# Optimization experiments

Hardware: AMD Instinct MI355X
Metric: run time of the kernel (lower is better)

The kernel has to match this reference:

```python
import jax, jax.numpy as jnp
import numpy as np
import math

K = 3
K2 = 9
BANDS = 8

def _linear(x, w, b):
    return x @ w.T + b

def _gelu(x):
    return jax.nn.gelu(x, approximate=False)

def setup_inputs() -> dict:
    key = jax.random.key(0)
    ks = jax.random.split(key, 14)
    def p(k, shape):
        return jax.random.normal(k, shape, dtype=jnp.float32) * 0.05
    inp = {
        "feat": jax.random.normal(ks[0], (2, 64, 128, 128), dtype=jnp.float32),
        "w1m": p(ks[1], (64, 85)),  "b1m": p(ks[2], (64,)),
        "w2m": p(ks[3], (64, 64)),  "b2m": p(ks[4], (64,)),
        "wk1": p(ks[5], (128, 640)), "bk1": p(ks[6], (128,)),
        "wk2": p(ks[7], (9, 128)),   "bk2": p(ks[8], (9,)),
        "wr1": p(ks[9], (64, 64)),   "br1": p(ks[10], (64,)),
        "wr2": p(ks[11], (3, 64)),   "br2": p(ks[12], (3,)),
        "scale": 2,
    }
    return inp

def reference(feat, w1m, b1m, w2m, b2m, wk1, bk1, wk2, bk2, wr1, br1, wr2, br2, scale):
    B, C, H, W = feat.shape
    s = float(scale)
    oh = max(1, int(round(H * s)))
    ow = max(1, int(round(W * s)))
    kappa = max(0.1, 1.0 / s)
    eta = min(1.0, 0.15 * s)
    pad = K // 2

    # ---- query geometry (shared across batch: uniform scale) ----
    ys = jnp.arange(oh, dtype=feat.dtype)
    xs = jnp.arange(ow, dtype=feat.dtype)
    yy, xx = jnp.meshgrid(ys, xs, indexing='ij')
    src_y = (yy + 0.5) / s - 0.5
    src_x = (xx + 0.5) / s - 0.5
    cell_y = jnp.floor(src_y)
    cell_x = jnp.floor(src_x)
    du = (src_x - cell_x - 0.5).reshape(-1)  # (q,)
    dv = (src_y - cell_y - 0.5).reshape(-1)
    q = oh * ow

    # ---- gather local KxK patches (replicates unfold + index_select) ----
    cy = jnp.clip(cell_y, 0, H - 1).astype(jnp.int32).reshape(-1)
    cx = jnp.clip(cell_x, 0, W - 1).astype(jnp.int32).reshape(-1)
    padded = jnp.pad(feat, ((0, 0), (0, 0), (pad, pad), (pad, pad)), mode='reflect')
    off = jnp.arange(K, dtype=jnp.int32)
    rows = cy[:, None] + off                 # (q, K) -> padded row indices
    cols = cx[:, None] + off                 # (q, K)
    # (B, C, q, K, K)
    g = padded[:, :, rows[:, :, None], cols[:, None, :]]
    g = jnp.transpose(g, (0, 2, 1, 3, 4)).reshape(B, q, C * K2)  # torch unfold layout (c, kh, kw)
    # torch does gathered.view(q, k2, c) on the channel-major flat -> faithful reshape
    patches = g.reshape(B, q, K2, C)
    patches_flat = g  # (B, q, C*K2), identical to patches.reshape(q, -1)

    # ---- meta fourier encoding + meta MLP (shared across batch) ----
    m = jnp.stack([
        jnp.full((q,), s, dtype=feat.dtype),
        du, dv,
        jnp.full((q,), kappa, dtype=feat.dtype),
        jnp.full((q,), eta, dtype=feat.dtype),
    ], axis=1)                               # (q, 5)
    freqs = (2.0 ** jnp.arange(BANDS, dtype=feat.dtype)) * math.pi
    xb = m[..., None] * freqs                # (q, 5, BANDS)
    enc = jnp.concatenate([m[..., None], jnp.sin(xb), jnp.cos(xb)], axis=-1).reshape(q, -1)  # (q, 85)
    m_emb = _linear(_gelu(_linear(enc, w1m, b1m)), w2m, b2m)  # (q, channels)

    # ---- kernel generation + softmax-weighted aggregate ----
    m_emb_b = jnp.broadcast_to(m_emb[None], (B, q, m_emb.shape[-1]))
    kin = jnp.concatenate([patches_flat, m_emb_b], axis=-1)   # (B, q, 640)
    weights = _linear(_gelu(_linear(kin, wk1, bk1)), wk2, bk2)  # (B, q, K2)
    weights = jax.nn.softmax(weights, axis=-1)
    f_q = jnp.einsum('bqk,bqkc->bqc', weights, patches)       # (B, q, C)

    # ---- rgb head ----
    rgb = _linear(_gelu(_linear(f_q, wr1, br1)), wr2, br2)    # (B, q, 3)
    rgb = rgb.reshape(B, oh, ow, -1).transpose(0, 3, 1, 2)    # (B, 3, oh, ow)
    return rgb
```

## Files before the change

### kernel.cpp

```cpp
#include <hip/hip_runtime.h>
#include <math.h>

#define HH 128
#define WW 128

typedef __attribute__((ext_vector_type(8))) short s16x8;
typedef __attribute__((ext_vector_type(8))) _Float16 h16x8;
typedef __attribute__((ext_vector_type(4))) float f32x4;

__device__ __forceinline__ float gelu_f(float x){
    return 0.5f * x * (1.0f + erff(x * 0.70710678118654752440f));
}
__device__ __forceinline__ float gelu2(float x){
    const float u2 = 1.5957691216057308f * x * (1.0f + 0.044715f * x * x);
    const float e  = __expf(u2);
    const float t  = 1.0f - 2.0f * __builtin_amdgcn_rcpf(e + 1.0f);
    return 0.5f * x * (1.0f + t);
}
__device__ __forceinline__ int refl(int v, int n){
    return v < 0 ? -v : (v >= n ? 2*n - 2 - v : v);
}
__device__ __forceinline__ ushort f2bf(float f){
    unsigned int b = __float_as_uint(f);
    unsigned int r = (b + 0x7FFFu + ((b >> 16) & 1u)) >> 16;
    return (ushort)r;
}
__device__ __forceinline__ float bf2f(ushort u){
    return __uint_as_float(((unsigned int)u) << 16);
}

__global__ __launch_bounds__(256) void featTp_kernel(
    const float* __restrict__ feat, ushort* __restrict__ featTp)
{
    __shared__ ushort tile[64*132];

    const int blk = blockIdx.x;
    const int b   = blk / 130;
    const int row = blk - b*130;
    const int sr  = refl(row - 1, HH);

    const int c2   = threadIdx.x >> 7;
    const int scol = threadIdx.x & 127;

    #pragma unroll 4
    for (int cc = 0; cc < 32; ++cc){
        const int c = cc*2 + c2;
        const float v = feat[(((size_t)(b*64 + c)) << 14) + (sr << 7) + scol];
        const ushort bv = f2bf(v);
        tile[c*132 + scol + 1] = bv;
        if (scol == 1)   tile[c*132 + 0]   = bv;
        if (scol == 126) tile[c*132 + 129] = bv;
    }
    __syncthreads();

    for (int e = threadIdx.x; e < 1040; e += 256){
        const int col = e >> 3;
        const int cb  = e & 7;
        ushort tmp[8];
        #pragma unroll
        for (int j = 0; j < 8; ++j) tmp[j] = tile[(cb*8 + j)*132 + col];
        *(int4*)(featTp + ((((size_t)b*130 + row)*130 + col) << 6) + cb*8)
            = *(const int4*)tmp;
    }
}

__global__ __launch_bounds__(256) void prep_all(
    const float* __restrict__ w1m, const float* __restrict__ b1m,
    const float* __restrict__ w2m, const float* __restrict__ b2m,
    const float* __restrict__ wk1, const float* __restrict__ bk1,
    const float* __restrict__ wr1,
    float* __restrict__ contrib, ushort* __restrict__ wk1tap,
    _Float16* __restrict__ wr1h)
{
    const int blk = blockIdx.x;
    const int t = threadIdx.x;

    if (blk == 0){
        __shared__ float hs[4][64];
        __shared__ float m_emb[4][64];
        const int p = t >> 6;
        const int j = t & 63;

        const float du = (p & 1) ? -0.25f : 0.25f;
        const float dv = (p >> 1) ? -0.25f : 0.25f;
        const float mv[5] = {2.0f, du, dv, 0.5f, 0.3f};

        float enc[85];
        #pragma unroll
        for (int f = 0; f < 5; ++f){
            enc[f*17] = mv[f];
            float fr = 3.14159265358979323846f;
            #pragma unroll
            for (int b = 0; b < 8; ++b){
                float xb = mv[f] * fr;
                enc[f*17 + 1 + b] = sinf(xb);
                enc[f*17 + 9 + b] = cosf(xb);
                fr *= 2.0f;
            }
        }

        float h = b1m[j];
        const float* __restrict__ wrow = w1m + j*85;
        #pragma unroll
        for (int i = 0; i < 85; ++i) h += enc[i] * wrow[i];
        hs[p][j] = gelu_f(h);
        __syncthreads();

        {
            const int o = j;
            float acc = b2m[o];
            const float* __restrict__ w2row = w2m + o*64;
            #pragma unroll
            for (int jj = 0; jj < 64; ++jj) acc += hs[p][jj] * w2row[jj];
            m_emb[p][o] = acc;
        }
        __syncthreads();

        for (int e = t; e < 512; e += 256){
            const int pp = e >> 7;
            const int oo = e & 127;
            float a = bk1[oo];
            #pragma unroll
            for (int jj = 0; jj < 64; ++jj) a += m_emb[pp][jj] * wk1[oo*640 + 576 + jj];
            contrib[e] = a;
        }
    } else if (blk <= 288){
        const int i = (blk - 1)*256 + t;
        if (i < 73728){
            const int c   = i & 63;
            const int o   = (i >> 6) & 127;
            const int tap = i >> 13;
            wk1tap[i] = f2bf(wk1[o*640 + c*9 + tap]);
        }
    } else {
        const int i = (blk - 289)*256 + t;
        if (i < 8192) wr1h[i] = (_Float16)wr1[i];
    }
}

__global__ __launch_bounds__(512) void conv_kernel(
    const ushort* __restrict__ featTp,
    const ushort* __restrict__ wk1tap,
    const float* __restrict__ wk2, const float* __restrict__ bk2,
    const float* __restrict__ contrib,
    _Float16* __restrict__ fqh)
{
    __shared__ ushort As[4*34*64];
    __shared__ ushort Ls16[64*130];
    __shared__ float  wk2t[128*12];
    __shared__ float  w9s[256*10];
    __shared__ float  contribs[512];

    const int t   = threadIdx.x;
    const int blk = blockIdx.x;
    const int b   = blk >> 8;
    const int rem = blk & 255;
    const int cy0 = (rem >> 2) * 2;
    const int cx0 = (rem & 3) * 32;

    for (int e = t; e < 1088; e += 512){
        const int r   = e / 272;
        const int rm  = e - r * 272;
        const int col = rm >> 3;
        const int cb  = rm & 7;
        const ushort* src = featTp + ((((size_t)b*130 + cy0 + r)*130 + cx0 + col) << 6) + cb*8;
        const int didx = (r*34 + col)*64 + ((cb ^ (col & 7)) << 3);
        *(int4*)&As[didx] = *(const int4*)src;
    }
    for (int e = t; e < 1536; e += 512){
        const int o = (e * 10923) >> 17;
        const int k = e - o*12;
        if (k < 9) wk2t[e] = wk2[k*128 + o];
    }
    if (t < 512) contribs[t] = contrib[t];
    __syncthreads();

    {
        const int lane = t & 63;
        const int w    = t >> 6;
        const int wn   = w & 1;
        const int wq   = w >> 1;
        const int cellrow = wq >> 1;
        const int colblk  = (wq & 1) * 16;
        const int l15  = lane & 15;
        const int l4   = lane >> 4;

        f32x4 acc[4];
        #pragma unroll
        for (int n = 0; n < 4; ++n) acc[n] = (f32x4){0.f,0.f,0.f,0.f};

        const int acol = colblk + l15;

        #pragma unroll
        for (int tap = 0; tap < 9; ++tap){
            const int ky = tap / 3;
            const int kx = tap - ky * 3;

            s16x8 bf[2][4];
            #pragma unroll
            for (int ks = 0; ks < 2; ++ks)
                #pragma unroll
                for (int n = 0; n < 4; ++n)
                    bf[ks][n] = *(const s16x8*)(wk1tap +
                        (((size_t)tap << 13) + ((wn*64 + n*16 + l15) << 6) + ks*32 + l4*8));

            const int col = acol + kx;
            const int rowbase = (cellrow + ky)*34 + col;
            const int sw = (col & 7);
            #pragma unroll
            for (int ks = 0; ks < 2; ++ks){
                const int cb0 = ks*4 + l4;
                const s16x8 af = *(const s16x8*)&As[rowbase*64 + ((cb0 ^ sw) << 3)];
                #pragma unroll
                for (int n = 0; n < 4; ++n)
                    acc[n] = __builtin_amdgcn_mfma_f32_16x16x32_bf16(af, bf[ks][n], acc[n], 0, 0, 0);
            }
        }

        #pragma unroll
        for (int n = 0; n < 4; ++n){
            #pragma unroll
            for (int reg = 0; reg < 4; ++reg){
                const int lc = cellrow*32 + colblk + l4*4 + reg;
                const int o  = wn*64 + n*16 + l15;
                Ls16[lc*130 + o] = __builtin_bit_cast(ushort, (_Float16)acc[n][reg]);
            }
        }
    }
    __syncthreads();

    if (t < 256){
        const int cell = t & 63;
        const int p    = t >> 6;

        float w9[9];
        #pragma unroll
        for (int k = 0; k < 9; ++k) w9[k] = 0.0f;

        const float* __restrict__ cp = contribs + p*128;
        for (int o = 0; o < 128; ++o){
            const float lv = (float)__builtin_bit_cast(_Float16, Ls16[cell*130 + o]);
            const float h  = gelu2(lv + cp[o]);
            const f32x4 wa = *(const f32x4*)&wk2t[o*12];
            const f32x4 wb = *(const f32x4*)&wk2t[o*12 + 4];
            w9[0] += h*wa[0]; w9[1] += h*wa[1]; w9[2] += h*wa[2]; w9[3] += h*wa[3];
            w9[4] += h*wb[0]; w9[5] += h*wb[1]; w9[6] += h*wb[2]; w9[7] += h*wb[3];
            w9[8] += h*wk2t[o*12 + 8];
        }
        #pragma unroll
        for (int k = 0; k < 9; ++k) w9[k] += bk2[k];

        float mx = w9[0];
        #pragma unroll
        for (int k = 1; k < 9; ++k) mx = fmaxf(mx, w9[k]);
        float sum = 0.0f;
        #pragma unroll
        for (int k = 0; k < 9; ++k){ w9[k] = __expf(w9[k] - mx); sum += w9[k]; }
        const float inv = __builtin_amdgcn_rcpf(sum);
        #pragma unroll
        for (int k = 0; k < 9; ++k) w9s[t*10 + k] = w9[k] * inv;
    }
    __syncthreads();

    {
        const int ci  = t >> 3;
        const int sub = t & 7;
        const int rr  = ci >> 5;
        const int x   = ci & 31;
        const int base_rc = rr*34 + x;
        const int c0 = sub*8;

        float w9r[4][9];
        #pragma unroll
        for (int p = 0; p < 4; ++p)
            #pragma unroll
            for (int k = 0; k < 9; ++k)
                w9r[p][k] = w9s[(p*64 + ci)*10 + k];

        float fqa[4][8];
        #pragma unroll
        for (int p = 0; p < 4; ++p)
            #pragma unroll
            for (int i = 0; i < 8; ++i) fqa[p][i] = 0.0f;

        #pragma unroll
        for (int k = 0; k < 9; ++k){
            #pragma unroll
            for (int i = 0; i < 8; ++i){
                const int e   = k*64 + c0 + i;
                const int ch  = (e * 7282) >> 16;
                const int tap = e - 9*ch;
                const int ty  = (tap * 11) >> 5;
                const int tx  = tap - 3*ty;
                const int col = x + tx;
                const int aidx = ((base_rc + ty*34 + tx) << 6)
                               + (((ch >> 3) ^ (col & 7)) << 3) + (ch & 7);
                const float v = bf2f(As[aidx]);
                fqa[0][i] += w9r[0][k] * v;
                fqa[1][i] += w9r[1][k] * v;
                fqa[2][i] += w9r[2][k] * v;
                fqa[3][i] += w9r[3][k] * v;
            }
        }

        const int gy = cy0 + rr;
        const int gx = cx0 + x;

        #pragma unroll
        for (int p = 0; p < 4; ++p){
            const int py = p >> 1, px = p & 1;
            h16x8 hv;
            #pragma unroll
            for (int i = 0; i < 8; ++i) hv[i] = (_Float16)fqa[p][i];

            const int oy0 = 2*gy + 2 - py;
            const int ox0 = 2*gx + 2 - px;
            const bool y0ok = (py == 1) || (gy < 127);
            const bool x0ok = (px == 1) || (gx < 127);
            const bool yEx  = (gy == 0) && (py == 0);
            const bool xEx  = (gx == 0) && (px == 0);

            if (y0ok && x0ok)
                *(h16x8*)(fqh + (((size_t)((b << 16) | (oy0 << 8) | ox0)) << 6) + c0) = hv;
            if (y0ok && xEx)
                *(h16x8*)(fqh + (((size_t)((b << 16) | (oy0 << 8))) << 6) + c0) = hv;
            if (yEx && x0ok)
                *(h16x8*)(fqh + (((size_t)((b << 16) | ox0)) << 6) + c0) = hv;
            if (yEx && xEx)
                *(h16x8*)(fqh + (((size_t)(b << 16)) << 6) + c0) = hv;
        }
    }
}

__global__ __launch_bounds__(256) void rgb_kernel(
    const _Float16* __restrict__ fqh,
    const _Float16* __restrict__ wr1h,
    const float* __restrict__ br1, const float* __restrict__ wr2,
    const float* __restrict__ br2,
    float* __restrict__ out)
{
    const int t    = threadIdx.x;
    const int w    = t >> 6;
    const int lane = t & 63;
    const int l15  = lane & 15;
    const int l4   = lane >> 4;
    const int rowbase = blockIdx.x*64 + w*16;

    const h16x8 a0 = *(const h16x8*)&fqh[(size_t)(rowbase + l15)*64 + l4*8];
    const h16x8 a1 = *(const h16x8*)&fqh[(size_t)(rowbase + l15)*64 + 32 + l4*8];

    f32x4 acc[4];
    #pragma unroll
    for (int n = 0; n < 4; ++n){
        const h16x8 b0 = *(const h16x8*)&wr1h[(n*16 + l15)*64 + l4*8];
        const h16x8 b1 = *(const h16x8*)&wr1h[(n*16 + l15)*64 + 32 + l4*8];
        acc[n] = (f32x4){0.f,0.f,0.f,0.f};
        acc[n] = __builtin_amdgcn_mfma_f32_16x16x32_f16(a0, b0, acc[n], 0, 0, 0);
        acc[n] = __builtin_amdgcn_mfma_f32_16x16x32_f16(a1, b1, acc[n], 0, 0, 0);
    }

    f32x4 br1v, wv0, wv1, wv2;
    #pragma unroll
    for (int n = 0; n < 4; ++n){
        const int col = n*16 + l15;
        br1v[n] = br1[col];
        wv0[n]  = wr2[col];
        wv1[n]  = wr2[64 + col];
        wv2[n]  = wr2[128 + col];
    }
    const float b2r0 = br2[0], b2r1 = br2[1], b2r2 = br2[2];

    #pragma unroll
    for (int reg = 0; reg < 4; ++reg){
        float r0 = 0.f, r1 = 0.f, r2 = 0.f;
        #pragma unroll
        for (int n = 0; n < 4; ++n){
            const float h = gelu2(acc[n][reg] + br1v[n]);
            r0 += h * wv0[n];
            r1 += h * wv1[n];
            r2 += h * wv2[n];
        }
        r0 += __shfl_xor(r0, 1); r0 += __shfl_xor(r0, 2); r0 += __shfl_xor(r0, 4); r0 += __shfl_xor(r0, 8);
        r1 += __shfl_xor(r1, 1); r1 += __shfl_xor(r1, 2); r1 += __shfl_xor(r1, 4); r1 += __shfl_xor(r1, 8);
        r2 += __shfl_xor(r2, 1); r2 += __shfl_xor(r2, 2); r2 += __shfl_xor(r2, 4); r2 += __shfl_xor(r2, 8);

        if (l15 == 0){
            const int row = rowbase + l4*4 + reg;
            const int b   = row >> 16;
            const int pix = row & 65535;
            out[((size_t)(b*3 + 0) << 16) + pix] = r0 + b2r0;
            out[((size_t)(b*3 + 1) << 16) + pix] = r1 + b2r1;
            out[((size_t)(b*3 + 2) << 16) + pix] = r2 + b2r2;
        }
    }
}

__global__ __launch_bounds__(256) void main_kernel_mono(
    const float* __restrict__ feat,
    const float* __restrict__ wk1,
    const float* __restrict__ wk2, const float* __restrict__ bk2,
    const float* __restrict__ wr1, const float* __restrict__ br1,
    const float* __restrict__ wr2, const float* __restrict__ br2,
    const float* __restrict__ contrib,
    float* __restrict__ out)
{
    const int tid = blockIdx.x * 256 + threadIdx.x;
    const int b  = tid >> 16;
    const int qi = tid & 65535;
    const int oy = qi >> 8;
    const int ox = qi & 255;

    int cy = (oy - 1) >> 1; if (cy < 0) cy = 0;
    int cx = (ox - 1) >> 1; if (cx < 0) cx = 0;

    int ry[3], rx[3];
    #pragma unroll
    for (int k = 0; k < 3; ++k){ ry[k] = refl(cy-1+k, HH); rx[k] = refl(cx-1+k, WW); }

    const int p = ((oy & 1) << 1) | (ox & 1);
    const float* __restrict__ fb = feat + ((size_t)b << 20);

    float w9[9];
    #pragma unroll
    for (int k = 0; k < 9; ++k) w9[k] = bk2[k];

    for (int oc = 0; oc < 4; ++oc){
        float acc[32];
        #pragma unroll
        for (int j = 0; j < 32; ++j) acc[j] = contrib[p*128 + oc*32 + j];
        for (int c = 0; c < 64; ++c){
            const float* __restrict__ fc = fb + c * (HH*WW);
            float v[9];
            #pragma unroll
            for (int ky = 0; ky < 3; ++ky){
                const float* __restrict__ frow = fc + ry[ky] * WW;
                #pragma unroll
                for (int kx = 0; kx < 3; ++kx) v[ky*3 + kx] = frow[rx[kx]];
            }
            const float* __restrict__ wrow0 = wk1 + (oc*32) * 640 + c * 9;
            #pragma unroll
            for (int j = 0; j < 32; ++j){
                const float* __restrict__ wrow = wrow0 + j * 640;
                float a = acc[j];
                #pragma unroll
                for (int kk = 0; kk < 9; ++kk) a += v[kk] * wrow[kk];
                acc[j] = a;
            }
        }
        #pragma unroll
        for (int j = 0; j < 32; ++j){
            const float h = gelu_f(acc[j]);
            const int o = oc*32 + j;
            #pragma unroll
            for (int k = 0; k < 9; ++k) w9[k] += h * wk2[k*128 + o];
        }
    }

    float mx = w9[0];
    #pragma unroll
    for (int k = 1; k < 9; ++k) mx = fmaxf(mx, w9[k]);
    float sum = 0.0f;
    #pragma unroll
    for (int k = 0; k < 9; ++k){ w9[k] = expf(w9[k] - mx); sum += w9[k]; }
    const float inv = 1.0f / sum;
    #pragma unroll
    for (int k = 0; k < 9; ++k) w9[k] *= inv;

    float fq[64];
    #pragma unroll
    for (int c = 0; c < 64; ++c){
        float a = 0.0f;
        #pragma unroll
        for (int k = 0; k < 9; ++k){
            const int j  = k*64 + c;
            const int ch = j / 9;
            const int kk = j % 9;
            a += w9[k] * fb[ch*(HH*WW) + ry[kk/3]*WW + rx[kk%3]];
        }
        fq[c] = a;
    }

    float r0 = br2[0], r1 = br2[1], r2 = br2[2];
    for (int o = 0; o < 64; ++o){
        float a = br1[o];
        #pragma unroll
        for (int c = 0; c < 64; ++c) a += fq[c] * wr1[o*64 + c];
        const float h = gelu_f(a);
        r0 += h * wr2[o];
        r1 += h * wr2[64 + o];
        r2 += h * wr2[128 + o];
    }

    const int pix = (oy << 8) | ox;
    out[((size_t)(b*3 + 0) << 16) + pix] = r0;
    out[((size_t)(b*3 + 1) << 16) + pix] = r1;
    out[((size_t)(b*3 + 2) << 16) + pix] = r2;
}

extern "C" void kernel_launch(void* const* d_in, const int* in_sizes, int n_in,
                              void* d_out, int out_size, void* d_ws, size_t ws_size,
                              hipStream_t stream)
{
    const float* feat = (const float*)d_in[0];
    const float* w1m  = (const float*)d_in[1];
    const float* b1m  = (const float*)d_in[2];
    const float* w2m  = (const float*)d_in[3];
    const float* b2m  = (const float*)d_in[4];
    const float* wk1  = (const float*)d_in[5];
    const float* bk1  = (const float*)d_in[6];
    const float* wk2  = (const float*)d_in[7];
    const float* bk2  = (const float*)d_in[8];
    const float* wr1  = (const float*)d_in[9];
    const float* br1  = (const float*)d_in[10];
    const float* wr2  = (const float*)d_in[11];
    const float* br2  = (const float*)d_in[12];

    float* out = (float*)d_out;

    char* ws = (char*)d_ws;
    float*     contrib = (float*)ws;
    ushort*    wk1tap  = (ushort*)(ws + 8192);
    _Float16*  wr1h    = (_Float16*)(ws + 155648);
    ushort*    featTp  = (ushort*)(ws + 172032);
    _Float16*  fqh     = (_Float16*)(ws + 4498432);
    const size_t need = 21275648;

    hipLaunchKernelGGL(prep_all, dim3(321), dim3(256), 0, stream,
                       w1m, b1m, w2m, b2m, wk1, bk1, wr1, contrib, wk1tap, wr1h);

    if (ws_size >= need){
        hipLaunchKernelGGL(featTp_kernel, dim3(260), dim3(256), 0, stream, feat, featTp);
        hipLaunchKernelGGL(conv_kernel, dim3(512), dim3(512), 0, stream,
                           featTp, wk1tap, wk2, bk2, contrib, fqh);
        hipLaunchKernelGGL(rgb_kernel, dim3(2048), dim3(256), 0, stream,
                           fqh, wr1h, br1, wr2, br2, out);
    } else {
        hipLaunchKernelGGL(main_kernel_mono, dim3(512), dim3(256), 0, stream,
                           feat, wk1, wk2, bk2, wr1, br1, wr2, br2, contrib, out);
    }
}
```

Measured before the change: 184.2 us.

## Merge feature transpose into prep kernel and halve conv tile per block

Folds the bf16 feature transpose into the prep_all launch as extra blocks, so one kernel launch and one dependency step go away. The conv kernel now covers 2x16 cells per block instead of 2x32, doubling the grid to 1024 blocks. The per-cell kernel-weight MLP is split across four threads per cell, with the partial sums combined by shuffles. Smaller tiles raise parallelism and occupancy through lower LDS use, but reload more halo and weights per output and add shuffle work.

```diff
diff --git a/kernel.cpp b/kernel.cpp
--- a/kernel.cpp
+++ b/kernel.cpp
@@ -29,49 +29,15 @@
     return __uint_as_float(((unsigned int)u) << 16);
 }
 
-__global__ __launch_bounds__(256) void featTp_kernel(
-    const float* __restrict__ feat, ushort* __restrict__ featTp)
-{
-    __shared__ ushort tile[64*132];
-
-    const int blk = blockIdx.x;
-    const int b   = blk / 130;
-    const int row = blk - b*130;
-    const int sr  = refl(row - 1, HH);
-
-    const int c2   = threadIdx.x >> 7;
-    const int scol = threadIdx.x & 127;
-
-    #pragma unroll 4
-    for (int cc = 0; cc < 32; ++cc){
-        const int c = cc*2 + c2;
-        const float v = feat[(((size_t)(b*64 + c)) << 14) + (sr << 7) + scol];
-        const ushort bv = f2bf(v);
-        tile[c*132 + scol + 1] = bv;
-        if (scol == 1)   tile[c*132 + 0]   = bv;
-        if (scol == 126) tile[c*132 + 129] = bv;
-    }
-    __syncthreads();
-
-    for (int e = threadIdx.x; e < 1040; e += 256){
-        const int col = e >> 3;
-        const int cb  = e & 7;
-        ushort tmp[8];
-        #pragma unroll
-        for (int j = 0; j < 8; ++j) tmp[j] = tile[(cb*8 + j)*132 + col];
-        *(int4*)(featTp + ((((size_t)b*130 + row)*130 + col) << 6) + cb*8)
-            = *(const int4*)tmp;
-    }
-}
-
 __global__ __launch_bounds__(256) void prep_all(
     const float* __restrict__ w1m, const float* __restrict__ b1m,
     const float* __restrict__ w2m, const float* __restrict__ b2m,
     const float* __restrict__ wk1, const float* __restrict__ bk1,
-    const float* __restrict__ wr1,
+    const float* __restrict__ wr1, const float* __restrict__ feat,
     float* __restrict__ contrib, ushort* __restrict__ wk1tap,
-    _Float16* __restrict__ wr1h)
+    _Float16* __restrict__ wr1h, ushort* __restrict__ featTp)
 {
+    __shared__ ushort tile[64*132];
     const int blk = blockIdx.x;
     const int t = threadIdx.x;
 
@@ -132,9 +98,38 @@
             const int tap = i >> 13;
             wk1tap[i] = f2bf(wk1[o*640 + c*9 + tap]);
         }
-    } else {
+    } else if (blk <= 320){
         const int i = (blk - 289)*256 + t;
         if (i < 8192) wr1h[i] = (_Float16)wr1[i];
+    } else {
+        const int rb  = blk - 321;
+        const int b   = rb / 130;
+        const int row = rb - b*130;
+        const int sr  = refl(row - 1, HH);
+
+        const int c2   = t >> 7;
+        const int scol = t & 127;
+
+        #pragma unroll 4
+        for (int cc = 0; cc < 32; ++cc){
+            const int c = cc*2 + c2;
+            const float v = feat[(((size_t)(b*64 + c)) << 14) + (sr << 7) + scol];
+            const ushort bv = f2bf(v);
+            tile[c*132 + scol + 1] = bv;
+            if (scol == 1)   tile[c*132 + 0]   = bv;
+            if (scol == 126) tile[c*132 + 129] = bv;
+        }
+        __syncthreads();
+
+        for (int e = t; e < 1040; e += 256){
+            const int col = e >> 3;
+            const int cb  = e & 7;
+            ushort tmp[8];
+            #pragma unroll
+            for (int j = 0; j < 8; ++j) tmp[j] = tile[(cb*8 + j)*132 + col];
+            *(int4*)(featTp + ((((size_t)b*130 + row)*130 + col) << 6) + cb*8)
+                = *(const int4*)tmp;
+        }
     }
 }
 
@@ -145,26 +140,26 @@
     const float* __restrict__ contrib,
     _Float16* __restrict__ fqh)
 {
-    __shared__ ushort As[4*34*64];
-    __shared__ ushort Ls16[64*130];
+    __shared__ ushort As[4*18*64];
+    __shared__ ushort Ls16[32*130];
     __shared__ float  wk2t[128*12];
-    __shared__ float  w9s[256*10];
+    __shared__ float  w9s[128*10];
     __shared__ float  contribs[512];
 
     const int t   = threadIdx.x;
     const int blk = blockIdx.x;
-    const int b   = blk >> 8;
-    const int rem = blk & 255;
-    const int cy0 = (rem >> 2) * 2;
-    const int cx0 = (rem & 3) * 32;
-
-    for (int e = t; e < 1088; e += 512){
-        const int r   = e / 272;
-        const int rm  = e - r * 272;
+    const int b   = blk >> 9;
+    const int rem = blk & 511;
+    const int cy0 = (rem >> 3) * 2;
+    const int cx0 = (rem & 7) * 16;
+
+    for (int e = t; e < 576; e += 512){
+        const int r   = e / 144;
+        const int rm  = e - r * 144;
         const int col = rm >> 3;
         const int cb  = rm & 7;
         const ushort* src = featTp + ((((size_t)b*130 + cy0 + r)*130 + cx0 + col) << 6) + cb*8;
-        const int didx = (r*34 + col)*64 + ((cb ^ (col & 7)) << 3);
+        const int didx = (r*18 + col)*64 + ((cb ^ (col & 7)) << 3);
         *(int4*)&As[didx] = *(const int4*)src;
     }
     for (int e = t; e < 1536; e += 512){
@@ -178,69 +173,69 @@
     {
         const int lane = t & 63;
         const int w    = t >> 6;
-        const int wn   = w & 1;
-        const int wq   = w >> 1;
-        const int cellrow = wq >> 1;
-        const int colblk  = (wq & 1) * 16;
+        const int wn   = w & 3;
+        const int cellrow = w >> 2;
         const int l15  = lane & 15;
         const int l4   = lane >> 4;
 
-        f32x4 acc[4];
-        #pragma unroll
-        for (int n = 0; n < 4; ++n) acc[n] = (f32x4){0.f,0.f,0.f,0.f};
-
-        const int acol = colblk + l15;
+        f32x4 acc[2];
+        acc[0] = (f32x4){0.f,0.f,0.f,0.f};
+        acc[1] = (f32x4){0.f,0.f,0.f,0.f};
 
         #pragma unroll
         for (int tap = 0; tap < 9; ++tap){
             const int ky = tap / 3;
             const int kx = tap - ky * 3;
 
-            s16x8 bf[2][4];
+            s16x8 bf[2][2];
             #pragma unroll
             for (int ks = 0; ks < 2; ++ks)
                 #pragma unroll
-                for (int n = 0; n < 4; ++n)
+                for (int n = 0; n < 2; ++n)
                     bf[ks][n] = *(const s16x8*)(wk1tap +
-                        (((size_t)tap << 13) + ((wn*64 + n*16 + l15) << 6) + ks*32 + l4*8));
-
-            const int col = acol + kx;
-            const int rowbase = (cellrow + ky)*34 + col;
+                        (((size_t)tap << 13) + ((wn*32 + n*16 + l15) << 6) + ks*32 + l4*8));
+
+            const int col = l15 + kx;
+            const int rowbase = (cellrow + ky)*18 + col;
             const int sw = (col & 7);
             #pragma unroll
             for (int ks = 0; ks < 2; ++ks){
                 const int cb0 = ks*4 + l4;
                 const s16x8 af = *(const s16x8*)&As[rowbase*64 + ((cb0 ^ sw) << 3)];
                 #pragma unroll
-                for (int n = 0; n < 4; ++n)
+                for (int n = 0; n < 2; ++n)
                     acc[n] = __builtin_amdgcn_mfma_f32_16x16x32_bf16(af, bf[ks][n], acc[n], 0, 0, 0);
             }
         }
 
         #pragma unroll
-        for (int n = 0; n < 4; ++n){
+        for (int n = 0; n < 2; ++n){
             #pragma unroll
             for (int reg = 0; reg < 4; ++reg){
-                const int lc = cellrow*32 + colblk + l4*4 + reg;
-                const int o  = wn*64 + n*16 + l15;
-                Ls16[lc*130 + o] = __builtin_bit_cast(ushort, (_Float16)acc[n][reg]);
+                const int cell = cellrow*16 + l4*4 + reg;
+                const int o    = wn*32 + n*16 + l15;
+                Ls16[cell*130 + o] = __builtin_bit_cast(ushort, (_Float16)acc[n][reg]);
             }
         }
     }
     __syncthreads();
 
-    if (t < 256){
-        const int cell = t & 63;
-        const int p    = t >> 6;
+    {
+        const int q    = t & 3;
+        const int task = t >> 2;
+        const int cell = task & 31;
+        const int p    = task >> 5;
 
         float w9[9];
         #pragma unroll
         for (int k = 0; k < 9; ++k) w9[k] = 0.0f;
 
-        const float* __restrict__ cp = contribs + p*128;
-        for (int o = 0; o < 128; ++o){
-            const float lv = (float)__builtin_bit_cast(_Float16, Ls16[cell*130 + o]);
-            const float h  = gelu2(lv + cp[o]);
+        const float* __restrict__ cp = contribs + p*128 + q*32;
+        const ushort* __restrict__ lp = &Ls16[cell*130 + q*32];
+        for (int i = 0; i < 32; ++i){
+            const float lv = (float)__builtin_bit_cast(_Float16, lp[i]);
+            const float h  = gelu2(lv + cp[i]);
+            const int o = q*32 + i;
             const f32x4 wa = *(const f32x4*)&wk2t[o*12];
             const f32x4 wb = *(const f32x4*)&wk2t[o*12 + 4];
             w9[0] += h*wa[0]; w9[1] += h*wa[1]; w9[2] += h*wa[2]; w9[3] += h*wa[3];
@@ -248,7 +243,11 @@
             w9[8] += h*wk2t[o*12 + 8];
         }
         #pragma unroll
-        for (int k = 0; k < 9; ++k) w9[k] += bk2[k];
+        for (int k = 0; k < 9; ++k){
+            w9[k] += __shfl_xor(w9[k], 1);
+            w9[k] += __shfl_xor(w9[k], 2);
+            w9[k] += bk2[k];
+        }
 
         float mx = w9[0];
         #pragma unroll
@@ -258,42 +257,43 @@
         for (int k = 0; k < 9; ++k){ w9[k] = __expf(w9[k] - mx); sum += w9[k]; }
         const float inv = __builtin_amdgcn_rcpf(sum);
         #pragma unroll
-        for (int k = 0; k < 9; ++k) w9s[t*10 + k] = w9[k] * inv;
+        for (int k = 0; k < 9; ++k)
+            if ((k & 3) == q) w9s[task*10 + k] = w9[k] * inv;
     }
     __syncthreads();
 
     {
-        const int ci  = t >> 3;
-        const int sub = t & 7;
-        const int rr  = ci >> 5;
-        const int x   = ci & 31;
-        const int base_rc = rr*34 + x;
-        const int c0 = sub*8;
+        const int ci  = t >> 4;
+        const int sub = t & 15;
+        const int rr  = ci >> 4;
+        const int x   = ci & 15;
+        const int base_rc = rr*18 + x;
+        const int c0 = sub*4;
 
         float w9r[4][9];
         #pragma unroll
         for (int p = 0; p < 4; ++p)
             #pragma unroll
             for (int k = 0; k < 9; ++k)
-                w9r[p][k] = w9s[(p*64 + ci)*10 + k];
-
-        float fqa[4][8];
+                w9r[p][k] = w9s[(p*32 + ci)*10 + k];
+
+        float fqa[4][4];
         #pragma unroll
         for (int p = 0; p < 4; ++p)
             #pragma unroll
-            for (int i = 0; i < 8; ++i) fqa[p][i] = 0.0f;
+            for (int i = 0; i < 4; ++i) fqa[p][i] = 0.0f;
 
         #pragma unroll
         for (int k = 0; k < 9; ++k){
             #pragma unroll
-            for (int i = 0; i < 8; ++i){
+            for (int i = 0; i < 4; ++i){
                 const int e   = k*64 + c0 + i;
                 const int ch  = (e * 7282) >> 16;
                 const int tap = e - 9*ch;
                 const int ty  = (tap * 11) >> 5;
                 const int tx  = tap - 3*ty;
                 const int col = x + tx;
-                const int aidx = ((base_rc + ty*34 + tx) << 6)
+                const int aidx = ((base_rc + ty*18 + tx) << 6)
                                + (((ch >> 3) ^ (col & 7)) << 3) + (ch & 7);
                 const float v = bf2f(As[aidx]);
                 fqa[0][i] += w9r[0][k] * v;
@@ -309,9 +309,11 @@
         #pragma unroll
         for (int p = 0; p < 4; ++p){
             const int py = p >> 1, px = p & 1;
-            h16x8 hv;
-            #pragma unroll
-            for (int i = 0; i < 8; ++i) hv[i] = (_Float16)fqa[p][i];
+            short4 hv;
+            hv.x = __builtin_bit_cast(short, (_Float16)fqa[p][0]);
+            hv.y = __builtin_bit_cast(short, (_Float16)fqa[p][1]);
+            hv.z = __builtin_bit_cast(short, (_Float16)fqa[p][2]);
+            hv.w = __builtin_bit_cast(short, (_Float16)fqa[p][3]);
 
             const int oy0 = 2*gy + 2 - py;
             const int ox0 = 2*gx + 2 - px;
@@ -321,13 +323,13 @@
             const bool xEx  = (gx == 0) && (px == 0);
 
             if (y0ok && x0ok)
-                *(h16x8*)(fqh + (((size_t)((b << 16) | (oy0 << 8) | ox0)) << 6) + c0) = hv;
+                *(short4*)(fqh + (((size_t)((b << 16) | (oy0 << 8) | ox0)) << 6) + c0) = hv;
             if (y0ok && xEx)
-                *(h16x8*)(fqh + (((size_t)((b << 16) | (oy0 << 8))) << 6) + c0) = hv;
+                *(short4*)(fqh + (((size_t)((b << 16) | (oy0 << 8))) << 6) + c0) = hv;
             if (yEx && x0ok)
-                *(h16x8*)(fqh + (((size_t)((b << 16) | ox0)) << 6) + c0) = hv;
+                *(short4*)(fqh + (((size_t)((b << 16) | ox0)) << 6) + c0) = hv;
             if (yEx && xEx)
-                *(h16x8*)(fqh + (((size_t)(b << 16)) << 6) + c0) = hv;
+                *(short4*)(fqh + (((size_t)(b << 16)) << 6) + c0) = hv;
         }
     }
 }
@@ -525,16 +527,18 @@
     _Float16*  fqh     = (_Float16*)(ws + 4498432);
     const size_t need = 21275648;
 
-    hipLaunchKernelGGL(prep_all, dim3(321), dim3(256), 0, stream,
-                       w1m, b1m, w2m, b2m, wk1, bk1, wr1, contrib, wk1tap, wr1h);
-
     if (ws_size >= need){
-        hipLaunchKernelGGL(featTp_kernel, dim3(260), dim3(256), 0, stream, feat, featTp);
-        hipLaunchKernelGGL(conv_kernel, dim3(512), dim3(512), 0, stream,
+        hipLaunchKernelGGL(prep_all, dim3(581), dim3(256), 0, stream,
+                           w1m, b1m, w2m, b2m, wk1, bk1, wr1, feat,
+                           contrib, wk1tap, wr1h, featTp);
+        hipLaunchKernelGGL(conv_kernel, dim3(1024), dim3(512), 0, stream,
                            featTp, wk1tap, wk2, bk2, contrib, fqh);
         hipLaunchKernelGGL(rgb_kernel, dim3(2048), dim3(256), 0, stream,
                            fqh, wr1h, br1, wr2, br2, out);
     } else {
+        hipLaunchKernelGGL(prep_all, dim3(321), dim3(256), 0, stream,
+                           w1m, b1m, w2m, b2m, wk1, bk1, wr1, feat,
+                           contrib, wk1tap, wr1h, featTp);
         hipLaunchKernelGGL(main_kernel_mono, dim3(512), dim3(256), 0, stream,
                            feat, wk1, wk2, bk2, wr1, br1, wr2, br2, contrib, out);
     }
```

Result: faster. 177.3 us (-3.7%).

## Fuse rgb head into conv kernel and fold feature transpose into prep

Applied to the files above, without the earlier changes.

The rgb MLP head now runs inside the conv kernel: per-query f16 features are staged in shared memory that aliases the now-idle Ls16/wk2t/contrib buffers, instead of being written to and re-read from a global fqh buffer. The feature transpose kernel is merged into prep_all as extra blocks. Together these remove a ~16MB global round trip and two kernel launches. In exchange the conv kernel does more work per block, adds a barrier, and the scattered output stores go through a single lane per 16 rows.

```diff
diff --git a/kernel.cpp b/kernel.cpp
--- a/kernel.cpp
+++ b/kernel.cpp
@@ -29,49 +29,15 @@
     return __uint_as_float(((unsigned int)u) << 16);
 }
 
-__global__ __launch_bounds__(256) void featTp_kernel(
-    const float* __restrict__ feat, ushort* __restrict__ featTp)
-{
-    __shared__ ushort tile[64*132];
-
-    const int blk = blockIdx.x;
-    const int b   = blk / 130;
-    const int row = blk - b*130;
-    const int sr  = refl(row - 1, HH);
-
-    const int c2   = threadIdx.x >> 7;
-    const int scol = threadIdx.x & 127;
-
-    #pragma unroll 4
-    for (int cc = 0; cc < 32; ++cc){
-        const int c = cc*2 + c2;
-        const float v = feat[(((size_t)(b*64 + c)) << 14) + (sr << 7) + scol];
-        const ushort bv = f2bf(v);
-        tile[c*132 + scol + 1] = bv;
-        if (scol == 1)   tile[c*132 + 0]   = bv;
-        if (scol == 126) tile[c*132 + 129] = bv;
-    }
-    __syncthreads();
-
-    for (int e = threadIdx.x; e < 1040; e += 256){
-        const int col = e >> 3;
-        const int cb  = e & 7;
-        ushort tmp[8];
-        #pragma unroll
-        for (int j = 0; j < 8; ++j) tmp[j] = tile[(cb*8 + j)*132 + col];
-        *(int4*)(featTp + ((((size_t)b*130 + row)*130 + col) << 6) + cb*8)
-            = *(const int4*)tmp;
-    }
-}
-
 __global__ __launch_bounds__(256) void prep_all(
     const float* __restrict__ w1m, const float* __restrict__ b1m,
     const float* __restrict__ w2m, const float* __restrict__ b2m,
     const float* __restrict__ wk1, const float* __restrict__ bk1,
-    const float* __restrict__ wr1,
+    const float* __restrict__ wr1, const float* __restrict__ feat,
     float* __restrict__ contrib, ushort* __restrict__ wk1tap,
-    _Float16* __restrict__ wr1h)
+    _Float16* __restrict__ wr1h, ushort* __restrict__ featTp)
 {
+    __shared__ ushort tile[64*132];
     const int blk = blockIdx.x;
     const int t = threadIdx.x;
 
@@ -132,24 +98,58 @@
             const int tap = i >> 13;
             wk1tap[i] = f2bf(wk1[o*640 + c*9 + tap]);
         }
-    } else {
+    } else if (blk <= 320){
         const int i = (blk - 289)*256 + t;
         if (i < 8192) wr1h[i] = (_Float16)wr1[i];
-    }
-}
-
-__global__ __launch_bounds__(512) void conv_kernel(
+    } else {
+        const int rb  = blk - 321;
+        const int b   = rb / 130;
+        const int row = rb - b*130;
+        const int sr  = refl(row - 1, HH);
+
+        const int c2   = t >> 7;
+        const int scol = t & 127;
+
+        #pragma unroll 4
+        for (int cc = 0; cc < 32; ++cc){
+            const int c = cc*2 + c2;
+            const float v = feat[(((size_t)(b*64 + c)) << 14) + (sr << 7) + scol];
+            const ushort bv = f2bf(v);
+            tile[c*132 + scol + 1] = bv;
+            if (scol == 1)   tile[c*132 + 0]   = bv;
+            if (scol == 126) tile[c*132 + 129] = bv;
+        }
+        __syncthreads();
+
+        for (int e = t; e < 1040; e += 256){
+            const int col = e >> 3;
+            const int cb  = e & 7;
+            ushort tmp[8];
+            #pragma unroll
+            for (int j = 0; j < 8; ++j) tmp[j] = tile[(cb*8 + j)*132 + col];
+            *(int4*)(featTp + ((((size_t)b*130 + row)*130 + col) << 6) + cb*8)
+                = *(const int4*)tmp;
+        }
+    }
+}
+
+__global__ __launch_bounds__(512) void conv_fused(
     const ushort* __restrict__ featTp,
     const ushort* __restrict__ wk1tap,
     const float* __restrict__ wk2, const float* __restrict__ bk2,
     const float* __restrict__ contrib,
-    _Float16* __restrict__ fqh)
+    const _Float16* __restrict__ wr1h,
+    const float* __restrict__ br1, const float* __restrict__ wr2,
+    const float* __restrict__ br2,
+    float* __restrict__ out)
 {
     __shared__ ushort As[4*34*64];
-    __shared__ ushort Ls16[64*130];
-    __shared__ float  wk2t[128*12];
     __shared__ float  w9s[256*10];
-    __shared__ float  contribs[512];
+    __shared__ __align__(16) char uB[34816];
+    ushort*   Ls16     = (ushort*)uB;
+    float*    wk2t     = (float*)(uB + 16640);
+    float*    contribs = (float*)(uB + 22784);
+    _Float16* fqs      = (_Float16*)uB;
 
     const int t   = threadIdx.x;
     const int blk = blockIdx.x;
@@ -172,7 +172,7 @@
         const int k = e - o*12;
         if (k < 9) wk2t[e] = wk2[k*128 + o];
     }
-    if (t < 512) contribs[t] = contrib[t];
+    contribs[t] = contrib[t & 511];
     __syncthreads();
 
     {
@@ -303,94 +303,99 @@
             }
         }
 
-        const int gy = cy0 + rr;
-        const int gx = cx0 + x;
-
         #pragma unroll
         for (int p = 0; p < 4; ++p){
-            const int py = p >> 1, px = p & 1;
             h16x8 hv;
             #pragma unroll
             for (int i = 0; i < 8; ++i) hv[i] = (_Float16)fqa[p][i];
-
-            const int oy0 = 2*gy + 2 - py;
-            const int ox0 = 2*gx + 2 - px;
-            const bool y0ok = (py == 1) || (gy < 127);
-            const bool x0ok = (px == 1) || (gx < 127);
-            const bool yEx  = (gy == 0) && (py == 0);
-            const bool xEx  = (gx == 0) && (px == 0);
-
-            if (y0ok && x0ok)
-                *(h16x8*)(fqh + (((size_t)((b << 16) | (oy0 << 8) | ox0)) << 6) + c0) = hv;
-            if (y0ok && xEx)
-                *(h16x8*)(fqh + (((size_t)((b << 16) | (oy0 << 8))) << 6) + c0) = hv;
-            if (yEx && x0ok)
-                *(h16x8*)(fqh + (((size_t)((b << 16) | ox0)) << 6) + c0) = hv;
-            if (yEx && xEx)
-                *(h16x8*)(fqh + (((size_t)(b << 16)) << 6) + c0) = hv;
-        }
-    }
-}
-
-__global__ __launch_bounds__(256) void rgb_kernel(
-    const _Float16* __restrict__ fqh,
-    const _Float16* __restrict__ wr1h,
-    const float* __restrict__ br1, const float* __restrict__ wr2,
-    const float* __restrict__ br2,
-    float* __restrict__ out)
-{
-    const int t    = threadIdx.x;
-    const int w    = t >> 6;
-    const int lane = t & 63;
-    const int l15  = lane & 15;
-    const int l4   = lane >> 4;
-    const int rowbase = blockIdx.x*64 + w*16;
-
-    const h16x8 a0 = *(const h16x8*)&fqh[(size_t)(rowbase + l15)*64 + l4*8];
-    const h16x8 a1 = *(const h16x8*)&fqh[(size_t)(rowbase + l15)*64 + 32 + l4*8];
-
-    f32x4 acc[4];
-    #pragma unroll
-    for (int n = 0; n < 4; ++n){
-        const h16x8 b0 = *(const h16x8*)&wr1h[(n*16 + l15)*64 + l4*8];
-        const h16x8 b1 = *(const h16x8*)&wr1h[(n*16 + l15)*64 + 32 + l4*8];
-        acc[n] = (f32x4){0.f,0.f,0.f,0.f};
-        acc[n] = __builtin_amdgcn_mfma_f32_16x16x32_f16(a0, b0, acc[n], 0, 0, 0);
-        acc[n] = __builtin_amdgcn_mfma_f32_16x16x32_f16(a1, b1, acc[n], 0, 0, 0);
-    }
-
-    f32x4 br1v, wv0, wv1, wv2;
-    #pragma unroll
-    for (int n = 0; n < 4; ++n){
-        const int col = n*16 + l15;
-        br1v[n] = br1[col];
-        wv0[n]  = wr2[col];
-        wv1[n]  = wr2[64 + col];
-        wv2[n]  = wr2[128 + col];
-    }
-    const float b2r0 = br2[0], b2r1 = br2[1], b2r2 = br2[2];
-
-    #pragma unroll
-    for (int reg = 0; reg < 4; ++reg){
-        float r0 = 0.f, r1 = 0.f, r2 = 0.f;
+            *(h16x8*)&fqs[(p*64 + ci)*68 + c0] = hv;
+        }
+    }
+    __syncthreads();
+
+    {
+        const int lane = t & 63;
+        const int w    = t >> 6;
+        const int l15  = lane & 15;
+        const int l4   = lane >> 4;
+
+        f32x4 br1v, wv0, wv1, wv2;
         #pragma unroll
         for (int n = 0; n < 4; ++n){
-            const float h = gelu2(acc[n][reg] + br1v[n]);
-            r0 += h * wv0[n];
-            r1 += h * wv1[n];
-            r2 += h * wv2[n];
-        }
-        r0 += __shfl_xor(r0, 1); r0 += __shfl_xor(r0, 2); r0 += __shfl_xor(r0, 4); r0 += __shfl_xor(r0, 8);
-        r1 += __shfl_xor(r1, 1); r1 += __shfl_xor(r1, 2); r1 += __shfl_xor(r1, 4); r1 += __shfl_xor(r1, 8);
-        r2 += __shfl_xor(r2, 1); r2 += __shfl_xor(r2, 2); r2 += __shfl_xor(r2, 4); r2 += __shfl_xor(r2, 8);
-
-        if (l15 == 0){
-            const int row = rowbase + l4*4 + reg;
-            const int b   = row >> 16;
-            const int pix = row & 65535;
-            out[((size_t)(b*3 + 0) << 16) + pix] = r0 + b2r0;
-            out[((size_t)(b*3 + 1) << 16) + pix] = r1 + b2r1;
-            out[((size_t)(b*3 + 2) << 16) + pix] = r2 + b2r2;
+            const int col = n*16 + l15;
+            br1v[n] = br1[col];
+            wv0[n]  = wr2[col];
+            wv1[n]  = wr2[64 + col];
+            wv2[n]  = wr2[128 + col];
+        }
+        const float b2r0 = br2[0], b2r1 = br2[1], b2r2 = br2[2];
+
+        #pragma unroll
+        for (int m2 = 0; m2 < 2; ++m2){
+            const int m   = w*2 + m2;
+            const int row = m*16 + l15;
+
+            const h16x8 a0 = *(const h16x8*)&fqs[row*68 + l4*8];
+            const h16x8 a1 = *(const h16x8*)&fqs[row*68 + 32 + l4*8];
+
+            f32x4 acc[4];
+            #pragma unroll
+            for (int n = 0; n < 4; ++n){
+                const h16x8 b0 = *(const h16x8*)&wr1h[(n*16 + l15)*64 + l4*8];
+                const h16x8 b1 = *(const h16x8*)&wr1h[(n*16 + l15)*64 + 32 + l4*8];
+                acc[n] = (f32x4){0.f,0.f,0.f,0.f};
+                acc[n] = __builtin_amdgcn_mfma_f32_16x16x32_f16(a0, b0, acc[n], 0, 0, 0);
+                acc[n] = __builtin_amdgcn_mfma_f32_16x16x32_f16(a1, b1, acc[n], 0, 0, 0);
+            }
+
+            #pragma unroll
+            for (int reg = 0; reg < 4; ++reg){
+                float r0 = 0.f, r1 = 0.f, r2 = 0.f;
+                #pragma unroll
+                for (int n = 0; n < 4; ++n){
+                    const float h = gelu2(acc[n][reg] + br1v[n]);
+                    r0 += h * wv0[n];
+                    r1 += h * wv1[n];
+                    r2 += h * wv2[n];
+                }
+                r0 += __shfl_xor(r0, 1); r0 += __shfl_xor(r0, 2); r0 += __shfl_xor(r0, 4); r0 += __shfl_xor(r0, 8);
+                r1 += __shfl_xor(r1, 1); r1 += __shfl_xor(r1, 2); r1 += __shfl_xor(r1, 4); r1 += __shfl_xor(r1, 8);
+                r2 += __shfl_xor(r2, 1); r2 += __shfl_xor(r2, 2); r2 += __shfl_xor(r2, 4); r2 += __shfl_xor(r2, 8);
+
+                if (l15 == 0){
+                    const int row2 = m*16 + l4*4 + reg;
+                    const int p    = row2 >> 6;
+                    const int cell = row2 & 63;
+                    const int gy = cy0 + (cell >> 5);
+                    const int gx = cx0 + (cell & 31);
+                    const int py = p >> 1, px = p & 1;
+
+                    const float v0 = r0 + b2r0, v1 = r1 + b2r1, v2 = r2 + b2r2;
+                    const int oy0 = 2*gy + 2 - py;
+                    const int ox0 = 2*gx + 2 - px;
+                    const bool y0ok = (py == 1) || (gy < 127);
+                    const bool x0ok = (px == 1) || (gx < 127);
+                    const bool yEx  = (gy == 0) && (py == 0);
+                    const bool xEx  = (gx == 0) && (px == 0);
+
+                    const size_t ob = ((size_t)b*3) << 16;
+                    if (y0ok && x0ok){
+                        const int pix = (oy0 << 8) | ox0;
+                        out[ob + pix] = v0; out[ob + 65536 + pix] = v1; out[ob + 131072 + pix] = v2;
+                    }
+                    if (y0ok && xEx){
+                        const int pix = (oy0 << 8);
+                        out[ob + pix] = v0; out[ob + 65536 + pix] = v1; out[ob + 131072 + pix] = v2;
+                    }
+                    if (yEx && x0ok){
+                        const int pix = ox0;
+                        out[ob + pix] = v0; out[ob + 65536 + pix] = v1; out[ob + 131072 + pix] = v2;
+                    }
+                    if (yEx && xEx){
+                        out[ob] = v0; out[ob + 65536] = v1; out[ob + 131072] = v2;
+                    }
+                }
+            }
         }
     }
 }
@@ -522,19 +527,19 @@
     ushort*    wk1tap  = (ushort*)(ws + 8192);
     _Float16*  wr1h    = (_Float16*)(ws + 155648);
     ushort*    featTp  = (ushort*)(ws + 172032);
-    _Float16*  fqh     = (_Float16*)(ws + 4498432);
-    const size_t need = 21275648;
-
-    hipLaunchKernelGGL(prep_all, dim3(321), dim3(256), 0, stream,
-                       w1m, b1m, w2m, b2m, wk1, bk1, wr1, contrib, wk1tap, wr1h);
+    const size_t need = 4498432;
 
     if (ws_size >= need){
-        hipLaunchKernelGGL(featTp_kernel, dim3(260), dim3(256), 0, stream, feat, featTp);
-        hipLaunchKernelGGL(conv_kernel, dim3(512), dim3(512), 0, stream,
-                           featTp, wk1tap, wk2, bk2, contrib, fqh);
-        hipLaunchKernelGGL(rgb_kernel, dim3(2048), dim3(256), 0, stream,
-                           fqh, wr1h, br1, wr2, br2, out);
+        hipLaunchKernelGGL(prep_all, dim3(581), dim3(256), 0, stream,
+                           w1m, b1m, w2m, b2m, wk1, bk1, wr1, feat,
+                           contrib, wk1tap, wr1h, featTp);
+        hipLaunchKernelGGL(conv_fused, dim3(512), dim3(512), 0, stream,
+                           featTp, wk1tap, wk2, bk2, contrib,
+                           wr1h, br1, wr2, br2, out);
     } else {
+        hipLaunchKernelGGL(prep_all, dim3(321), dim3(256), 0, stream,
+                           w1m, b1m, w2m, b2m, wk1, bk1, wr1, feat,
+                           contrib, wk1tap, wr1h, featTp);
         hipLaunchKernelGGL(main_kernel_mono, dim3(512), dim3(256), 0, stream,
                            feat, wk1, wk2, bk2, wr1, br1, wr2, br2, contrib, out);
     }
```

Measured after the change: 176.0 us. -4.4%, faster.
